# Kernel tuning notes

Measured on AMD Instinct MI355X. Metric: run time of the kernel, lower is better.

The kernel has to match this reference:

```python
import jax, jax.numpy as jnp
import numpy as np
from jax import lax

B, NM, P, F, E, H, K = 32, 131072, 256, 3, 64, 4, 3
DH = E // H


def layer_norm(x, gamma, beta, eps=1e-5):
    mu = x.mean(-1, keepdims=True)
    var = ((x - mu) ** 2).mean(-1, keepdims=True)
    return (x - mu) * lax.rsqrt(var + eps) * gamma + beta


def knn_interp(x, pos_x, pos_y, k=K):
    """x: [B, Nx, F] features at pos_x [Nx, 2]; interpolate to pos_y [Ny, 2].
    Positions are shared across the batch (they are tiled in the torch code),
    so KNN indices/weights are computed once. Matches torch knn + inverse-
    squared-distance weighted scatter (uniform per-batch counts => gather form).
    """
    d2 = jnp.sum((pos_y[:, None, :] - pos_x[None, :, :]) ** 2, axis=-1)  # [Ny, Nx]
    neg_d2, idx = lax.top_k(-d2, k)                                      # [Ny, k]
    w = 1.0 / jnp.clip(-neg_d2, 1e-16)                                   # [Ny, k]
    w = lax.stop_gradient(w)  # torch computes weights under no_grad
    gathered = x[:, idx, :]                                              # [B, Ny, k, F]
    num = jnp.sum(gathered * w[None, :, :, None], axis=2)                # [B, Ny, F]
    den = jnp.sum(w, axis=1)[None, :, None]                              # [1, Ny, 1]
    return num / den


def setup_inputs() -> dict:
    key = jax.random.key(0)
    ks = jax.random.split(key, 8)
    return {
        "node_attr": jax.random.normal(ks[0], (B * NM, F), jnp.float32),
        "position_mesh": jax.random.uniform(ks[1], (NM, 2), jnp.float32),
        "position_pivotal": jax.random.uniform(ks[2], (P, 2), jnp.float32),
        "ln_gamma": jnp.ones((F,), jnp.float32),
        "ln_beta": jnp.zeros((F,), jnp.float32),
        "Wf": jax.random.normal(ks[3], (E, F), jnp.float32) * (2.0 / E) ** 0.5,
        "bf": jnp.zeros((E,), jnp.float32),
        "Wp": jax.random.normal(ks[4], (E, 2), jnp.float32) * (2.0 / E) ** 0.5,
        "bp": jnp.zeros((E,), jnp.float32),
        "in_proj_w": jax.random.normal(ks[5], (3 * E, E), jnp.float32) * (1.0 / E) ** 0.5,
        "in_proj_b": jnp.zeros((3 * E,), jnp.float32),
        "batch_size": B,
    }


def reference(node_attr, position_mesh, position_pivotal, ln_gamma, ln_beta,
              Wf, bf, Wp, bp, in_proj_w, in_proj_b, batch_size):
    x = node_attr.reshape(batch_size, -1, F)                 # [B, NM, F]
    # PivotalNorm after encoder (encoder/decoder MeshGraphNet omitted: undefined dep)
    x = layer_norm(x, ln_gamma, ln_beta)
    # ---- downsample: mesh -> pivotal via inverse-distance KNN interpolation ----
    y = knn_interp(x, position_mesh, position_pivotal)       # [B, P, F]
    # attention-based pooling over pivotal nodes
    q = (jnp.einsum('bpf,ef->bpe', y, Wf) + bf
         + (position_pivotal @ Wp.T + bp)[None])             # [B, P, E]
    Wq, Wk = in_proj_w[:E], in_proj_w[E:2 * E]
    bq, bk = in_proj_b[:E], in_proj_b[E:2 * E]
    Q = (q @ Wq.T + bq).reshape(batch_size, P, H, DH)
    Kt = (q @ Wk.T + bk).reshape(batch_size, P, H, DH)
    scores = jnp.einsum('bqhd,bkhd->bhqk', Q, Kt) / np.float32(np.sqrt(DH))
    attn = jax.nn.softmax(scores, axis=-1)                   # [B, H, P, P]
    attn_w = attn.mean(axis=1)                               # avg heads, [B, P, P]
    y = jnp.einsum('bqk,bkf->bqf', attn_w, y)                # [B, P, F]
    # ---- interpolate: pivotal -> mesh ----
    out = knn_interp(y, position_pivotal, position_mesh)     # [B, NM, F]
    return out.reshape(-1, F)
```

## Files before the change

kernel.cpp:

```cpp
#include <hip/hip_runtime.h>
#include <math.h>

#define NM 131072
#define PP 256
#define BB 32

#define INF_F 3.0e38f
#define LDW 13

#define KA_BLOCKS 256
#define KB_BLOCKS 512

__device__ __forceinline__ void ins3(float d, int i,
    float& d0, float& d1, float& d2, int& i0, int& i1, int& i2) {
  bool l0 = d < d0, l1 = d < d1, l2 = d < d2;
  d2 = l1 ? d1 : (l2 ? d : d2);
  i2 = l1 ? i1 : (l2 ? i : i2);
  d1 = l0 ? d0 : (l1 ? d : d1);
  i1 = l0 ? i0 : (l1 ? i : i1);
  d0 = l0 ? d : d0;
  i0 = l0 ? i : i0;
}

__device__ __forceinline__ bool lt2(float d, int i, float D, int I) {
  return (d < D) || (d == D && i < I);
}

__device__ __forceinline__ void ins3t(float d, int i,
    float& d0, float& d1, float& d2, int& i0, int& i1, int& i2) {
  bool l0 = lt2(d, i, d0, i0), l1 = lt2(d, i, d1, i1), l2 = lt2(d, i, d2, i2);
  d2 = l1 ? d1 : (l2 ? d : d2);
  i2 = l1 ? i1 : (l2 ? i : i2);
  d1 = l0 ? d0 : (l1 ? d : d1);
  i1 = l0 ? i0 : (l1 ? i : i1);
  d0 = l0 ? d : d0;
  i0 = l0 ? i : i0;
}

__device__ __forceinline__ float dist2(float ax, float ay, float bx, float by) {
  float dx = ax - bx, dy = ay - by;
  return __fadd_rn(__fmul_rn(dx, dx), __fmul_rn(dy, dy));
}

__global__ __launch_bounds__(1024)
void fused_knn(const float* __restrict__ mesh, const float* __restrict__ piv,
               float* __restrict__ wA, int* __restrict__ idxA,
               float* __restrict__ wB, int* __restrict__ idxB,
               float* __restrict__ y2) {
  const int blk = blockIdx.x;
  const int tid = threadIdx.x;
  __shared__ float sdf[PP * LDW];
  __shared__ int   sif[PP * LDW];

  if (blk < KA_BLOCKS) {
    const int p = blk;
    const float2 pv = ((const float2*)piv)[p];
    const float2* m2 = (const float2*)mesh;
    float d0 = INF_F, d1 = INF_F, d2 = INF_F;
    int i0 = 0, i1 = 0, i2 = 0;
#pragma unroll 4
    for (int j = 0; j < 128; ++j) {
      int idx = tid + (j << 10);
      float2 mp = m2[idx];
      ins3(dist2(pv.x, pv.y, mp.x, mp.y), idx, d0, d1, d2, i0, i1, i2);
    }
    sdf[tid * 3 + 0] = d0; sif[tid * 3 + 0] = i0;
    sdf[tid * 3 + 1] = d1; sif[tid * 3 + 1] = i1;
    sdf[tid * 3 + 2] = d2; sif[tid * 3 + 2] = i2;
    __syncthreads();

    if (tid < 128) {
      float e0 = INF_F, e1 = INF_F, e2 = INF_F; int j0 = 0, j1 = 0, j2 = 0;
#pragma unroll
      for (int s = 0; s < 8; ++s) {
        int o = (tid + 128 * s) * 3;
#pragma unroll
        for (int k = 0; k < 3; ++k) ins3t(sdf[o + k], sif[o + k], e0, e1, e2, j0, j1, j2);
      }
      sdf[tid * 3 + 0] = e0; sif[tid * 3 + 0] = j0;
      sdf[tid * 3 + 1] = e1; sif[tid * 3 + 1] = j1;
      sdf[tid * 3 + 2] = e2; sif[tid * 3 + 2] = j2;
    }
    __syncthreads();

    if (tid < 16) {
      float e0 = INF_F, e1 = INF_F, e2 = INF_F; int j0 = 0, j1 = 0, j2 = 0;
#pragma unroll
      for (int s = 0; s < 8; ++s) {
        int o = (tid + 16 * s) * 3;
#pragma unroll
        for (int k = 0; k < 3; ++k) ins3t(sdf[o + k], sif[o + k], e0, e1, e2, j0, j1, j2);
      }
      sdf[tid * 3 + 0] = e0; sif[tid * 3 + 0] = j0;
      sdf[tid * 3 + 1] = e1; sif[tid * 3 + 1] = j1;
      sdf[tid * 3 + 2] = e2; sif[tid * 3 + 2] = j2;
    }
    __syncthreads();

    if (tid == 0) {
      float e0 = INF_F, e1 = INF_F, e2 = INF_F; int j0 = 0, j1 = 0, j2 = 0;
      for (int s = 0; s < 16; ++s) {
        int o = s * 3;
#pragma unroll
        for (int k = 0; k < 3; ++k) ins3t(sdf[o + k], sif[o + k], e0, e1, e2, j0, j1, j2);
      }
      wA[p * 3 + 0] = 1.0f / fmaxf(e0, 1e-16f); idxA[p * 3 + 0] = j0;
      wA[p * 3 + 1] = 1.0f / fmaxf(e1, 1e-16f); idxA[p * 3 + 1] = j1;
      wA[p * 3 + 2] = 1.0f / fmaxf(e2, 1e-16f); idxA[p * 3 + 2] = j2;
    }
  } else if (blk < KA_BLOCKS + KB_BLOCKS) {
    const int bi = blk - KA_BLOCKS;
    const int ml = tid & 255;
    const int sub = tid >> 8;
    const int m = bi * 256 + ml;
    const float2 mv = ((const float2*)mesh)[m];
    float d0 = INF_F, d1 = INF_F, d2 = INF_F;
    int i0 = 0, i1 = 0, i2 = 0;
    const int base = sub * 64;
#pragma unroll 4
    for (int i = 0; i < 64; ++i) {
      int idx = base + i;
      float px = piv[2 * idx], py = piv[2 * idx + 1];
      ins3(dist2(mv.x, mv.y, px, py), idx, d0, d1, d2, i0, i1, i2);
    }
    sdf[ml * LDW + sub * 3 + 0] = d0; sif[ml * LDW + sub * 3 + 0] = i0;
    sdf[ml * LDW + sub * 3 + 1] = d1; sif[ml * LDW + sub * 3 + 1] = i1;
    sdf[ml * LDW + sub * 3 + 2] = d2; sif[ml * LDW + sub * 3 + 2] = i2;
    __syncthreads();

    if (tid < 256) {
      float e0 = sdf[tid * LDW + 0], e1 = sdf[tid * LDW + 1], e2 = sdf[tid * LDW + 2];
      int j0 = sif[tid * LDW + 0], j1 = sif[tid * LDW + 1], j2 = sif[tid * LDW + 2];
#pragma unroll
      for (int s = 1; s < 4; ++s)
#pragma unroll
        for (int k = 0; k < 3; ++k)
          ins3(sdf[tid * LDW + s * 3 + k], sif[tid * LDW + s * 3 + k], e0, e1, e2, j0, j1, j2);
      const int m0 = bi * 256 + tid;
      wB[m0 * 3 + 0] = 1.0f / fmaxf(e0, 1e-16f); idxB[m0 * 3 + 0] = j0;
      wB[m0 * 3 + 1] = 1.0f / fmaxf(e1, 1e-16f); idxB[m0 * 3 + 1] = j1;
      wB[m0 * 3 + 2] = 1.0f / fmaxf(e2, 1e-16f); idxB[m0 * 3 + 2] = j2;
    }
  } else {
    float4 z; z.x = 0.f; z.y = 0.f; z.z = 0.f; z.w = 0.f;
    float4* p4 = (float4*)y2;
#pragma unroll
    for (int j = 0; j < 6; ++j) p4[tid + (j << 10)] = z;
  }
}

__global__ __launch_bounds__(128, 2)
void gather_qqk(const float* __restrict__ node, const float* __restrict__ piv,
                const float* __restrict__ gamma, const float* __restrict__ beta,
                const float* __restrict__ Wf, const float* __restrict__ bf,
                const float* __restrict__ Wp, const float* __restrict__ bp,
                const float* __restrict__ ipw, const float* __restrict__ ipb,
                const float* __restrict__ wA, const int* __restrict__ idxA,
                float* __restrict__ y, float* __restrict__ Qh, float* __restrict__ Kh) {
  const int b = blockIdx.x >> 5;
  const int ptile = (blockIdx.x & 31) * 8;
  const int t = threadIdx.x;
  __shared__ float qs[8][64];
  __shared__ float ys[8][3];

  if (t < 8) {
    const int p = ptile + t;
    const float g0 = gamma[0], g1 = gamma[1], g2 = gamma[2];
    const float be0 = beta[0], be1 = beta[1], be2 = beta[2];
    float num0 = 0.f, num1 = 0.f, num2 = 0.f, den = 0.f;
#pragma unroll
    for (int k = 0; k < 3; ++k) {
      int idx = idxA[p * 3 + k];
      float w = wA[p * 3 + k];
      const float* r = node + ((size_t)b * NM + idx) * 3;
      float a0 = r[0], a1 = r[1], a2 = r[2];
      float mu = (a0 + a1 + a2) * (1.0f / 3.0f);
      float e0 = a0 - mu, e1 = a1 - mu, e2 = a2 - mu;
      float var = (e0 * e0 + e1 * e1 + e2 * e2) * (1.0f / 3.0f);
      float sc = 1.0f / sqrtf(var + 1e-5f);
      num0 += (e0 * sc * g0 + be0) * w;
      num1 += (e1 * sc * g1 + be1) * w;
      num2 += (e2 * sc * g2 + be2) * w;
      den += w;
    }
    float o0 = num0 / den, o1 = num1 / den, o2 = num2 / den;
    ys[t][0] = o0; ys[t][1] = o1; ys[t][2] = o2;
    float* yr = y + (b * PP + p) * 3;
    yr[0] = o0; yr[1] = o1; yr[2] = o2;
  }
  __syncthreads();

  const int e = t & 63;
  const int half = t >> 6;
  {
    float wf0 = Wf[e * 3], wf1 = Wf[e * 3 + 1], wf2 = Wf[e * 3 + 2];
    float wp0 = Wp[e * 2], wp1 = Wp[e * 2 + 1];
    float cst = bf[e] + bp[e];
    for (int r = half; r < 8; r += 2) {
      int p = ptile + r;
      float pe = piv[2 * p] * wp0 + piv[2 * p + 1] * wp1;
      qs[r][e] = ys[r][0] * wf0 + ys[r][1] * wf1 + ys[r][2] * wf2 + cst + pe;
    }
  }
  __syncthreads();

  const int row = half * 64 + e;
  float wreg[64];
  const float4* W4 = (const float4*)(ipw + row * 64);
#pragma unroll
  for (int j = 0; j < 16; ++j) {
    float4 v = W4[j];
    wreg[4 * j] = v.x; wreg[4 * j + 1] = v.y; wreg[4 * j + 2] = v.z; wreg[4 * j + 3] = v.w;
  }
  float bias = ipb[row];
  float* dst = half ? Kh : Qh;
  const int h = e >> 4, d = e & 15;
  for (int r = 0; r < 8; ++r) {
    float acc = bias;
#pragma unroll
    for (int j = 0; j < 64; ++j) acc += qs[r][j] * wreg[j];
    int p = ptile + r;
    dst[(((b * 4 + h) * PP) + p) * 16 + d] = acc;
  }
}

__global__ void attn_kernel(const float* __restrict__ Qh, const float* __restrict__ Kh,
                            const float* __restrict__ y, float* __restrict__ y2) {
  const int b = blockIdx.x >> 3;
  const int h = (blockIdx.x >> 1) & 3;
  const int qh = blockIdx.x & 1;
  const int t = threadIdx.x;
  const int q = qh * 128 + t;

  __shared__ float Ks[PP * 16];
  __shared__ float ys[PP * 3];

  {
    const float4* src = (const float4*)(Kh + (size_t)(b * 4 + h) * PP * 16);
    float4* dst = (float4*)Ks;
#pragma unroll
    for (int j = 0; j < 8; ++j) dst[j * 128 + t] = src[j * 128 + t];
    const float* ysrc = y + b * PP * 3;
#pragma unroll
    for (int j = 0; j < 6; ++j) ys[j * 128 + t] = ysrc[j * 128 + t];
  }
  __syncthreads();

  const float4* q4 = (const float4*)(Qh + ((size_t)((b * 4 + h) * PP) + q) * 16);
  float4 qa = q4[0], qb = q4[1], qc = q4[2], qd = q4[3];

  float m = -INF_F, l = 0.f, a0 = 0.f, a1 = 0.f, a2 = 0.f;
#pragma unroll 4
  for (int k = 0; k < PP; ++k) {
    const float4* kr = (const float4*)(Ks + k * 16);
    float4 k0 = kr[0], k1 = kr[1], k2 = kr[2], k3 = kr[3];
    float dot = qa.x * k0.x + qa.y * k0.y + qa.z * k0.z + qa.w * k0.w
              + qb.x * k1.x + qb.y * k1.y + qb.z * k1.z + qb.w * k1.w
              + qc.x * k2.x + qc.y * k2.y + qc.z * k2.z + qc.w * k2.w
              + qd.x * k3.x + qd.y * k3.y + qd.z * k3.z + qd.w * k3.w;
    float s = dot * 0.25f;
    float mn = fmaxf(m, s);
    float p = __expf(s - mn);
    float sc = __expf(m - mn);
    float y0 = ys[k * 3], y1 = ys[k * 3 + 1], yy2 = ys[k * 3 + 2];
    l = l * sc + p;
    a0 = a0 * sc + p * y0;
    a1 = a1 * sc + p * y1;
    a2 = a2 * sc + p * yy2;
    m = mn;
  }
  float inv = 0.25f / l;
  float* o = y2 + (b * PP + q) * 3;
  atomicAdd(o + 0, a0 * inv);
  atomicAdd(o + 1, a1 * inv);
  atomicAdd(o + 2, a2 * inv);
}

__global__ __launch_bounds__(256)
void interp_out(const float* __restrict__ wB, const int* __restrict__ idxB,
                const float* __restrict__ y2, float* __restrict__ out) {
  const int tid = threadIdx.x;
  const int ml = tid & 63;
  const int sub = tid >> 6;
  const int m = blockIdx.x * 64 + ml;

  const float w0 = wB[m * 3 + 0], w1 = wB[m * 3 + 1], w2 = wB[m * 3 + 2];
  const int o0 = idxB[m * 3 + 0] * 3, o1 = idxB[m * 3 + 1] * 3, o2 = idxB[m * 3 + 2] * 3;
  const float inv = 1.0f / (w0 + w1 + w2);

#pragma unroll 2
  for (int bi = 0; bi < 8; ++bi) {
    const int b = sub * 8 + bi;
    const float* yb = y2 + b * PP * 3;
    float3 r0 = *(const float3*)(yb + o0);
    float3 r1 = *(const float3*)(yb + o1);
    float3 r2 = *(const float3*)(yb + o2);
    float3 res;
    res.x = (w0 * r0.x + w1 * r1.x + w2 * r2.x) * inv;
    res.y = (w0 * r0.y + w1 * r1.y + w2 * r2.y) * inv;
    res.z = (w0 * r0.z + w1 * r1.z + w2 * r2.z) * inv;
    *(float3*)(out + ((size_t)b * NM + m) * 3) = res;
  }
}

extern "C" void kernel_launch(void* const* d_in, const int* in_sizes, int n_in,
                              void* d_out, int out_size, void* d_ws, size_t ws_size,
                              hipStream_t stream) {
  const float* node  = (const float*)d_in[0];
  const float* mesh  = (const float*)d_in[1];
  const float* piv   = (const float*)d_in[2];
  const float* gamma = (const float*)d_in[3];
  const float* beta  = (const float*)d_in[4];
  const float* Wf    = (const float*)d_in[5];
  const float* bf    = (const float*)d_in[6];
  const float* Wp    = (const float*)d_in[7];
  const float* bp    = (const float*)d_in[8];
  const float* ipw   = (const float*)d_in[9];
  const float* ipb   = (const float*)d_in[10];
  float* out = (float*)d_out;

  float* wA   = (float*)d_ws;
  int*   idxA = (int*)(wA + PP * 3);
  float* y    = (float*)(idxA + PP * 3);
  float* Qh   = y + BB * PP * 3;
  float* Kh   = Qh + BB * PP * 64;
  float* y2   = Kh + BB * PP * 64;
  float* wB   = y2 + BB * PP * 3;
  int*   idxB = (int*)(wB + NM * 3);

  fused_knn<<<KA_BLOCKS + KB_BLOCKS + 1, 1024, 0, stream>>>(mesh, piv, wA, idxA, wB, idxB, y2);
  gather_qqk<<<BB * 32, 128, 0, stream>>>(node, piv, gamma, beta, Wf, bf, Wp, bp, ipw, ipb,
                                          wA, idxA, y, Qh, Kh);
  attn_kernel<<<BB * 4 * 2, 128, 0, stream>>>(Qh, Kh, y, y2);
  interp_out<<<NM / 64, 256, 0, stream>>>(wB, idxB, y2, out);
}
```

Baseline: 199.4 us.

## Replace brute-force KNN with uniform-grid bucketing and ring search

Replaces the brute-force KNN searches with uniform spatial grids. Mesh points go into a 64x64 grid and pivotal points into a 16x16 grid, each with an overflow list, and queries expand ring by ring until the third-nearest distance is bounded. The mesh-to-pivotal KNN is fused into the output interpolation kernel, removing the wB/idxB workspace round-trip, and attention's online softmax is split into four independent chains for more instruction-level parallelism. It adds a memset, atomic bucket-building and data-dependent control flow. Tie-breaking now relies on packed 64-bit keys.

```diff
diff --git a/kernel.cpp b/kernel.cpp
--- a/kernel.cpp
+++ b/kernel.cpp
@@ -4,37 +4,26 @@
 #define NM 131072
 #define PP 256
 #define BB 32
-
 #define INF_F 3.0e38f
-#define LDW 13
-
-#define KA_BLOCKS 256
-#define KB_BLOCKS 512
-
-__device__ __forceinline__ void ins3(float d, int i,
-    float& d0, float& d1, float& d2, int& i0, int& i1, int& i2) {
-  bool l0 = d < d0, l1 = d < d1, l2 = d < d2;
-  d2 = l1 ? d1 : (l2 ? d : d2);
-  i2 = l1 ? i1 : (l2 ? i : i2);
-  d1 = l0 ? d0 : (l1 ? d : d1);
-  i1 = l0 ? i0 : (l1 ? i : i1);
-  d0 = l0 ? d : d0;
-  i0 = l0 ? i : i0;
-}
-
-__device__ __forceinline__ bool lt2(float d, int i, float D, int I) {
-  return (d < D) || (d == D && i < I);
-}
-
-__device__ __forceinline__ void ins3t(float d, int i,
-    float& d0, float& d1, float& d2, int& i0, int& i1, int& i2) {
-  bool l0 = lt2(d, i, d0, i0), l1 = lt2(d, i, d1, i1), l2 = lt2(d, i, d2, i2);
-  d2 = l1 ? d1 : (l2 ? d : d2);
-  i2 = l1 ? i1 : (l2 ? i : i2);
-  d1 = l0 ? d0 : (l1 ? d : d1);
-  i1 = l0 ? i0 : (l1 ? i : i1);
-  d0 = l0 ? d : d0;
-  i0 = l0 ? i : i0;
+
+#define GM   64
+#define GM2  (GM * GM)
+#define CAPM 96
+#define GP   16
+#define GP2  (GP * GP)
+#define CAPP 8
+
+typedef unsigned long long u64;
+
+__device__ __forceinline__ u64 packkey(float d, int i) {
+  return ((u64)__float_as_uint(d) << 32) | (unsigned)i;
+}
+
+__device__ __forceinline__ void ins3k(u64 k, u64& k0, u64& k1, u64& k2) {
+  bool l0 = k < k0, l1 = k < k1, l2 = k < k2;
+  k2 = l1 ? k1 : (l2 ? k : k2);
+  k1 = l0 ? k0 : (l1 ? k : k1);
+  k0 = l0 ? k : k0;
 }
 
 __device__ __forceinline__ float dist2(float ax, float ay, float bx, float by) {
@@ -42,110 +31,157 @@
   return __fadd_rn(__fmul_rn(dx, dx), __fmul_rn(dy, dy));
 }
 
-__global__ __launch_bounds__(1024)
-void fused_knn(const float* __restrict__ mesh, const float* __restrict__ piv,
-               float* __restrict__ wA, int* __restrict__ idxA,
-               float* __restrict__ wB, int* __restrict__ idxB,
-               float* __restrict__ y2) {
-  const int blk = blockIdx.x;
-  const int tid = threadIdx.x;
-  __shared__ float sdf[PP * LDW];
-  __shared__ int   sif[PP * LDW];
-
-  if (blk < KA_BLOCKS) {
-    const int p = blk;
-    const float2 pv = ((const float2*)piv)[p];
-    const float2* m2 = (const float2*)mesh;
-    float d0 = INF_F, d1 = INF_F, d2 = INF_F;
-    int i0 = 0, i1 = 0, i2 = 0;
-#pragma unroll 4
-    for (int j = 0; j < 128; ++j) {
-      int idx = tid + (j << 10);
-      float2 mp = m2[idx];
-      ins3(dist2(pv.x, pv.y, mp.x, mp.y), idx, d0, d1, d2, i0, i1, i2);
-    }
-    sdf[tid * 3 + 0] = d0; sif[tid * 3 + 0] = i0;
-    sdf[tid * 3 + 1] = d1; sif[tid * 3 + 1] = i1;
-    sdf[tid * 3 + 2] = d2; sif[tid * 3 + 2] = i2;
+__global__ __launch_bounds__(256)
+void build_buckets(const float* __restrict__ mesh, const float* __restrict__ piv,
+                   unsigned* __restrict__ cntM, unsigned* __restrict__ cntP,
+                   unsigned* __restrict__ ovfc,
+                   float* __restrict__ bufM,
+                   int* __restrict__ bufP,
+                   float* __restrict__ ovfM, int* __restrict__ ovfP,
+                   float* __restrict__ y2) {
+  const int g = blockIdx.x * 256 + threadIdx.x;
+  if (g < NM) {
+    float2 mp = ((const float2*)mesh)[g];
+    int cx = min((int)(mp.x * GM), GM - 1);
+    int cy = min((int)(mp.y * GM), GM - 1);
+    int c = cy * GM + cx;
+    unsigned s = atomicAdd(&cntM[c], 1u);
+    if (s < CAPM) {
+      float* d = bufM + (size_t)(c * CAPM + s) * 3;
+      d[0] = mp.x; d[1] = mp.y; ((int*)d)[2] = g;
+    } else {
+      unsigned o = atomicAdd(&ovfc[0], 1u);
+      float* d = ovfM + (size_t)o * 3;
+      d[0] = mp.x; d[1] = mp.y; ((int*)d)[2] = g;
+    }
+  }
+  if (blockIdx.x == 0 && threadIdx.x < PP) {
+    const int p = threadIdx.x;
+    float2 pv = ((const float2*)piv)[p];
+    int cx = min((int)(pv.x * GP), GP - 1);
+    int cy = min((int)(pv.y * GP), GP - 1);
+    int c = cy * GP + cx;
+    unsigned s = atomicAdd(&cntP[c], 1u);
+    if (s < CAPP) bufP[c * CAPP + s] = p;
+    else { unsigned o = atomicAdd(&ovfc[1], 1u); ovfP[o] = p; }
+  }
+  if (blockIdx.x == 1) {
+    for (int j = threadIdx.x; j < BB * PP * 3; j += 256) y2[j] = 0.f;
+  }
+}
+
+__global__ __launch_bounds__(256)
+void knnA_grid(const float* __restrict__ piv,
+               const unsigned* __restrict__ cntM, const float* __restrict__ bufM,
+               const unsigned* __restrict__ ovfc, const float* __restrict__ ovfM,
+               float* __restrict__ wA, int* __restrict__ idxA) {
+  const int p = blockIdx.x;
+  const int t = threadIdx.x;
+  __shared__ u64 sk[256 * 3];
+  __shared__ u64 g3[3];
+  __shared__ int sdone;
+
+  const float2 pv = ((const float2*)piv)[p];
+  const int cx = min((int)(pv.x * GM), GM - 1);
+  const int cy = min((int)(pv.y * GM), GM - 1);
+
+  u64 b0 = ~0ull, b1 = ~0ull, b2 = ~0ull;
+
+  {
+    int x0 = max(cx - 1, 0), x1 = min(cx + 1, GM - 1);
+    int y0 = max(cy - 1, 0), y1 = min(cy + 1, GM - 1);
+    for (int yy = y0; yy <= y1; ++yy) {
+      int cb = yy * GM + x0;
+      int tot = (x1 - x0 + 1) * CAPM;
+      for (int s = t; s < tot; s += 256) {
+        int ci = s / CAPM, j = s - ci * CAPM;
+        int c = cb + ci;
+        if (j < (int)min(cntM[c], (unsigned)CAPM)) {
+          const float* cp = bufM + (size_t)(c * CAPM + j) * 3;
+          float d = dist2(pv.x, pv.y, cp[0], cp[1]);
+          ins3k(packkey(d, ((const int*)cp)[2]), b0, b1, b2);
+        }
+      }
+    }
+    int no = (int)ovfc[0];
+    for (int j = t; j < no; j += 256) {
+      const float* cp = ovfM + (size_t)j * 3;
+      float d = dist2(pv.x, pv.y, cp[0], cp[1]);
+      ins3k(packkey(d, ((const int*)cp)[2]), b0, b1, b2);
+    }
+  }
+
+  int R = 1;
+  u64 p0 = ~0ull, p1 = ~0ull, p2 = ~0ull;
+  while (true) {
+    sk[t * 3 + 0] = b0; sk[t * 3 + 1] = b1; sk[t * 3 + 2] = b2;
     __syncthreads();
-
-    if (tid < 128) {
-      float e0 = INF_F, e1 = INF_F, e2 = INF_F; int j0 = 0, j1 = 0, j2 = 0;
+    if (t < 32) {
+      u64 e0 = ~0ull, e1 = ~0ull, e2 = ~0ull;
 #pragma unroll
       for (int s = 0; s < 8; ++s) {
-        int o = (tid + 128 * s) * 3;
-#pragma unroll
-        for (int k = 0; k < 3; ++k) ins3t(sdf[o + k], sif[o + k], e0, e1, e2, j0, j1, j2);
-      }
-      sdf[tid * 3 + 0] = e0; sif[tid * 3 + 0] = j0;
-      sdf[tid * 3 + 1] = e1; sif[tid * 3 + 1] = j1;
-      sdf[tid * 3 + 2] = e2; sif[tid * 3 + 2] = j2;
+        int o = (t + 32 * s) * 3;
+        ins3k(sk[o], e0, e1, e2); ins3k(sk[o + 1], e0, e1, e2); ins3k(sk[o + 2], e0, e1, e2);
+      }
+      sk[t * 3] = e0; sk[t * 3 + 1] = e1; sk[t * 3 + 2] = e2;
     }
     __syncthreads();
-
-    if (tid < 16) {
-      float e0 = INF_F, e1 = INF_F, e2 = INF_F; int j0 = 0, j1 = 0, j2 = 0;
-#pragma unroll
-      for (int s = 0; s < 8; ++s) {
-        int o = (tid + 16 * s) * 3;
-#pragma unroll
-        for (int k = 0; k < 3; ++k) ins3t(sdf[o + k], sif[o + k], e0, e1, e2, j0, j1, j2);
-      }
-      sdf[tid * 3 + 0] = e0; sif[tid * 3 + 0] = j0;
-      sdf[tid * 3 + 1] = e1; sif[tid * 3 + 1] = j1;
-      sdf[tid * 3 + 2] = e2; sif[tid * 3 + 2] = j2;
+    if (t == 0) {
+      u64 e0 = p0, e1 = p1, e2 = p2;
+      for (int s = 0; s < 32; ++s) {
+        ins3k(sk[s * 3], e0, e1, e2); ins3k(sk[s * 3 + 1], e0, e1, e2); ins3k(sk[s * 3 + 2], e0, e1, e2);
+      }
+      g3[0] = e0; g3[1] = e1; g3[2] = e2;
+      float d2f = __uint_as_float((unsigned)(e2 >> 32));
+      float md = (float)R * (1.0f / GM);
+      sdone = (md * md > d2f) ? 1 : 0;
     }
     __syncthreads();
-
-    if (tid == 0) {
-      float e0 = INF_F, e1 = INF_F, e2 = INF_F; int j0 = 0, j1 = 0, j2 = 0;
-      for (int s = 0; s < 16; ++s) {
-        int o = s * 3;
-#pragma unroll
-        for (int k = 0; k < 3; ++k) ins3t(sdf[o + k], sif[o + k], e0, e1, e2, j0, j1, j2);
-      }
-      wA[p * 3 + 0] = 1.0f / fmaxf(e0, 1e-16f); idxA[p * 3 + 0] = j0;
-      wA[p * 3 + 1] = 1.0f / fmaxf(e1, 1e-16f); idxA[p * 3 + 1] = j1;
-      wA[p * 3 + 2] = 1.0f / fmaxf(e2, 1e-16f); idxA[p * 3 + 2] = j2;
-    }
-  } else if (blk < KA_BLOCKS + KB_BLOCKS) {
-    const int bi = blk - KA_BLOCKS;
-    const int ml = tid & 255;
-    const int sub = tid >> 8;
-    const int m = bi * 256 + ml;
-    const float2 mv = ((const float2*)mesh)[m];
-    float d0 = INF_F, d1 = INF_F, d2 = INF_F;
-    int i0 = 0, i1 = 0, i2 = 0;
-    const int base = sub * 64;
-#pragma unroll 4
-    for (int i = 0; i < 64; ++i) {
-      int idx = base + i;
-      float px = piv[2 * idx], py = piv[2 * idx + 1];
-      ins3(dist2(mv.x, mv.y, px, py), idx, d0, d1, d2, i0, i1, i2);
-    }
-    sdf[ml * LDW + sub * 3 + 0] = d0; sif[ml * LDW + sub * 3 + 0] = i0;
-    sdf[ml * LDW + sub * 3 + 1] = d1; sif[ml * LDW + sub * 3 + 1] = i1;
-    sdf[ml * LDW + sub * 3 + 2] = d2; sif[ml * LDW + sub * 3 + 2] = i2;
+    if (sdone) break;
+    p0 = g3[0]; p1 = g3[1]; p2 = g3[2];
+    b0 = b1 = b2 = ~0ull;
+    R += 1;
+    int x0 = max(cx - R, 0), x1 = min(cx + R, GM - 1);
+    for (int pass = 0; pass < 2; ++pass) {
+      int yy = pass ? cy + R : cy - R;
+      if (yy < 0 || yy > GM - 1) continue;
+      int cb = yy * GM + x0;
+      int tot = (x1 - x0 + 1) * CAPM;
+      for (int s = t; s < tot; s += 256) {
+        int ci = s / CAPM, j = s - ci * CAPM;
+        int c = cb + ci;
+        if (j < (int)min(cntM[c], (unsigned)CAPM)) {
+          const float* cp = bufM + (size_t)(c * CAPM + j) * 3;
+          float d = dist2(pv.x, pv.y, cp[0], cp[1]);
+          ins3k(packkey(d, ((const int*)cp)[2]), b0, b1, b2);
+        }
+      }
+    }
+    int yy0 = max(cy - R + 1, 0), yy1 = min(cy + R - 1, GM - 1);
+    for (int pass = 0; pass < 2; ++pass) {
+      int xx = pass ? cx + R : cx - R;
+      if (xx < 0 || xx > GM - 1) continue;
+      int tot = (yy1 - yy0 + 1) * CAPM;
+      for (int s = t; s < tot; s += 256) {
+        int ri = s / CAPM, j = s - ri * CAPM;
+        int c = (yy0 + ri) * GM + xx;
+        if (j < (int)min(cntM[c], (unsigned)CAPM)) {
+          const float* cp = bufM + (size_t)(c * CAPM + j) * 3;
+          float d = dist2(pv.x, pv.y, cp[0], cp[1]);
+          ins3k(packkey(d, ((const int*)cp)[2]), b0, b1, b2);
+        }
+      }
+    }
     __syncthreads();
-
-    if (tid < 256) {
-      float e0 = sdf[tid * LDW + 0], e1 = sdf[tid * LDW + 1], e2 = sdf[tid * LDW + 2];
-      int j0 = sif[tid * LDW + 0], j1 = sif[tid * LDW + 1], j2 = sif[tid * LDW + 2];
-#pragma unroll
-      for (int s = 1; s < 4; ++s)
-#pragma unroll
-        for (int k = 0; k < 3; ++k)
-          ins3(sdf[tid * LDW + s * 3 + k], sif[tid * LDW + s * 3 + k], e0, e1, e2, j0, j1, j2);
-      const int m0 = bi * 256 + tid;
-      wB[m0 * 3 + 0] = 1.0f / fmaxf(e0, 1e-16f); idxB[m0 * 3 + 0] = j0;
-      wB[m0 * 3 + 1] = 1.0f / fmaxf(e1, 1e-16f); idxB[m0 * 3 + 1] = j1;
-      wB[m0 * 3 + 2] = 1.0f / fmaxf(e2, 1e-16f); idxB[m0 * 3 + 2] = j2;
-    }
-  } else {
-    float4 z; z.x = 0.f; z.y = 0.f; z.z = 0.f; z.w = 0.f;
-    float4* p4 = (float4*)y2;
-#pragma unroll
-    for (int j = 0; j < 6; ++j) p4[tid + (j << 10)] = z;
+  }
+  if (t == 0) {
+#pragma unroll
+    for (int k = 0; k < 3; ++k) {
+      u64 e = g3[k];
+      float d = __uint_as_float((unsigned)(e >> 32));
+      wA[p * 3 + k] = 1.0f / fmaxf(d, 1e-16f);
+      idxA[p * 3 + k] = (int)(unsigned)(e & 0xffffffffu);
+    }
   }
 }
 
@@ -234,7 +270,6 @@
 
   __shared__ float Ks[PP * 16];
   __shared__ float ys[PP * 3];
-
   {
     const float4* src = (const float4*)(Kh + (size_t)(b * 4 + h) * PP * 16);
     float4* dst = (float4*)Ks;
@@ -249,52 +284,148 @@
   const float4* q4 = (const float4*)(Qh + ((size_t)((b * 4 + h) * PP) + q) * 16);
   float4 qa = q4[0], qb = q4[1], qc = q4[2], qd = q4[3];
 
-  float m = -INF_F, l = 0.f, a0 = 0.f, a1 = 0.f, a2 = 0.f;
-#pragma unroll 4
-  for (int k = 0; k < PP; ++k) {
-    const float4* kr = (const float4*)(Ks + k * 16);
-    float4 k0 = kr[0], k1 = kr[1], k2 = kr[2], k3 = kr[3];
-    float dot = qa.x * k0.x + qa.y * k0.y + qa.z * k0.z + qa.w * k0.w
-              + qb.x * k1.x + qb.y * k1.y + qb.z * k1.z + qb.w * k1.w
-              + qc.x * k2.x + qc.y * k2.y + qc.z * k2.z + qc.w * k2.w
-              + qd.x * k3.x + qd.y * k3.y + qd.z * k3.z + qd.w * k3.w;
-    float s = dot * 0.25f;
-    float mn = fmaxf(m, s);
-    float p = __expf(s - mn);
-    float sc = __expf(m - mn);
-    float y0 = ys[k * 3], y1 = ys[k * 3 + 1], yy2 = ys[k * 3 + 2];
-    l = l * sc + p;
-    a0 = a0 * sc + p * y0;
-    a1 = a1 * sc + p * y1;
-    a2 = a2 * sc + p * yy2;
-    m = mn;
-  }
+  float m0 = -INF_F, m1 = -INF_F, m2 = -INF_F, m3 = -INF_F;
+  float l0 = 0, l1 = 0, l2 = 0, l3 = 0;
+  float a00 = 0, a01 = 0, a02 = 0, a10 = 0, a11 = 0, a12 = 0;
+  float a20 = 0, a21 = 0, a22 = 0, a30 = 0, a31 = 0, a32 = 0;
+
+#define CHAIN(c, mC, lC, aC0, aC1, aC2) { \
+    int k = (c) * 64 + kk; \
+    const float4* kr = (const float4*)(Ks + k * 16); \
+    float4 K0 = kr[0], K1 = kr[1], K2 = kr[2], K3 = kr[3]; \
+    float dot = qa.x*K0.x + qa.y*K0.y + qa.z*K0.z + qa.w*K0.w \
+              + qb.x*K1.x + qb.y*K1.y + qb.z*K1.z + qb.w*K1.w \
+              + qc.x*K2.x + qc.y*K2.y + qc.z*K2.z + qc.w*K2.w \
+              + qd.x*K3.x + qd.y*K3.y + qd.z*K3.z + qd.w*K3.w; \
+    float s = dot * 0.25f; \
+    float mn = fmaxf(mC, s); \
+    float pE = __expf(s - mn); \
+    float sc = __expf(mC - mn); \
+    float yv0 = ys[k * 3], yv1 = ys[k * 3 + 1], yv2 = ys[k * 3 + 2]; \
+    lC = lC * sc + pE; \
+    aC0 = aC0 * sc + pE * yv0; \
+    aC1 = aC1 * sc + pE * yv1; \
+    aC2 = aC2 * sc + pE * yv2; \
+    mC = mn; }
+
+#pragma unroll 2
+  for (int kk = 0; kk < 64; ++kk) {
+    CHAIN(0, m0, l0, a00, a01, a02)
+    CHAIN(1, m1, l1, a10, a11, a12)
+    CHAIN(2, m2, l2, a20, a21, a22)
+    CHAIN(3, m3, l3, a30, a31, a32)
+  }
+#undef CHAIN
+
+  float M = fmaxf(fmaxf(m0, m1), fmaxf(m2, m3));
+  float e0 = __expf(m0 - M), e1 = __expf(m1 - M), e2 = __expf(m2 - M), e3 = __expf(m3 - M);
+  float l = l0 * e0 + l1 * e1 + l2 * e2 + l3 * e3;
+  float A0 = a00 * e0 + a10 * e1 + a20 * e2 + a30 * e3;
+  float A1 = a01 * e0 + a11 * e1 + a21 * e2 + a31 * e3;
+  float A2 = a02 * e0 + a12 * e1 + a22 * e2 + a32 * e3;
   float inv = 0.25f / l;
   float* o = y2 + (b * PP + q) * 3;
-  atomicAdd(o + 0, a0 * inv);
-  atomicAdd(o + 1, a1 * inv);
-  atomicAdd(o + 2, a2 * inv);
+  atomicAdd(o + 0, A0 * inv);
+  atomicAdd(o + 1, A1 * inv);
+  atomicAdd(o + 2, A2 * inv);
 }
 
 __global__ __launch_bounds__(256)
-void interp_out(const float* __restrict__ wB, const int* __restrict__ idxB,
-                const float* __restrict__ y2, float* __restrict__ out) {
-  const int tid = threadIdx.x;
-  const int ml = tid & 63;
-  const int sub = tid >> 6;
-  const int m = blockIdx.x * 64 + ml;
-
-  const float w0 = wB[m * 3 + 0], w1 = wB[m * 3 + 1], w2 = wB[m * 3 + 2];
-  const int o0 = idxB[m * 3 + 0] * 3, o1 = idxB[m * 3 + 1] * 3, o2 = idxB[m * 3 + 2] * 3;
-  const float inv = 1.0f / (w0 + w1 + w2);
-
-#pragma unroll 2
-  for (int bi = 0; bi < 8; ++bi) {
-    const int b = sub * 8 + bi;
+void interp_knnB_out(const float* __restrict__ mesh, const float* __restrict__ piv,
+                     const unsigned* __restrict__ cntP, const int* __restrict__ bufP,
+                     const unsigned* __restrict__ ovfc, const int* __restrict__ ovfP,
+                     const float* __restrict__ y2, float* __restrict__ out) {
+  const int t = threadIdx.x;
+  __shared__ float spx[PP], spy[PP];
+  __shared__ unsigned scnt[GP2];
+  __shared__ int sbuf[GP2 * CAPP];
+  {
+    float2 pvv = ((const float2*)piv)[t];
+    spx[t] = pvv.x; spy[t] = pvv.y;
+    scnt[t] = cntP[t];
+    for (int j = t; j < GP2 * CAPP; j += 256) sbuf[j] = bufP[j];
+  }
+  __syncthreads();
+
+  const int m = blockIdx.x * 256 + t;
+  const float2 mv = ((const float2*)mesh)[m];
+  const int cx = min((int)(mv.x * GP), GP - 1);
+  const int cy = min((int)(mv.y * GP), GP - 1);
+  u64 k0 = ~0ull, k1 = ~0ull, k2 = ~0ull;
+
+  {
+    int x0 = max(cx - 2, 0), x1 = min(cx + 2, GP - 1);
+    int y0 = max(cy - 2, 0), y1 = min(cy + 2, GP - 1);
+    for (int yy = y0; yy <= y1; ++yy)
+      for (int xx = x0; xx <= x1; ++xx) {
+        int c = yy * GP + xx;
+        int n = (int)min(scnt[c], (unsigned)CAPP);
+        for (int j = 0; j < n; ++j) {
+          int qq = sbuf[c * CAPP + j];
+          float d = dist2(mv.x, mv.y, spx[qq], spy[qq]);
+          ins3k(packkey(d, qq), k0, k1, k2);
+        }
+      }
+    int no = (int)ovfc[1];
+    for (int j = 0; j < no; ++j) {
+      int qq = ovfP[j];
+      float d = dist2(mv.x, mv.y, spx[qq], spy[qq]);
+      ins3k(packkey(d, qq), k0, k1, k2);
+    }
+  }
+  int R = 2;
+  while (true) {
+    float d2f = __uint_as_float((unsigned)(k2 >> 32));
+    float md = (float)R * (1.0f / GP);
+    if (md * md > d2f) break;
+    R += 1;
+    if (R >= 2 * GP) break;
+    int x0 = max(cx - R, 0), x1 = min(cx + R, GP - 1);
+    for (int pass = 0; pass < 2; ++pass) {
+      int yy = pass ? cy + R : cy - R;
+      if (yy < 0 || yy > GP - 1) continue;
+      for (int xx = x0; xx <= x1; ++xx) {
+        int c = yy * GP + xx;
+        int n = (int)min(scnt[c], (unsigned)CAPP);
+        for (int j = 0; j < n; ++j) {
+          int qq = sbuf[c * CAPP + j];
+          float d = dist2(mv.x, mv.y, spx[qq], spy[qq]);
+          ins3k(packkey(d, qq), k0, k1, k2);
+        }
+      }
+    }
+    int yy0 = max(cy - R + 1, 0), yy1 = min(cy + R - 1, GP - 1);
+    for (int pass = 0; pass < 2; ++pass) {
+      int xx = pass ? cx + R : cx - R;
+      if (xx < 0 || xx > GP - 1) continue;
+      for (int yy = yy0; yy <= yy1; ++yy) {
+        int c = yy * GP + xx;
+        int n = (int)min(scnt[c], (unsigned)CAPP);
+        for (int j = 0; j < n; ++j) {
+          int qq = sbuf[c * CAPP + j];
+          float d = dist2(mv.x, mv.y, spx[qq], spy[qq]);
+          ins3k(packkey(d, qq), k0, k1, k2);
+        }
+      }
+    }
+  }
+
+  float d0 = __uint_as_float((unsigned)(k0 >> 32));
+  float d1 = __uint_as_float((unsigned)(k1 >> 32));
+  float d2v = __uint_as_float((unsigned)(k2 >> 32));
+  int j0 = (int)(unsigned)(k0 & 0xffffffffu) * 3;
+  int j1 = (int)(unsigned)(k1 & 0xffffffffu) * 3;
+  int j2 = (int)(unsigned)(k2 & 0xffffffffu) * 3;
+  float w0 = 1.0f / fmaxf(d0, 1e-16f);
+  float w1 = 1.0f / fmaxf(d1, 1e-16f);
+  float w2 = 1.0f / fmaxf(d2v, 1e-16f);
+  float inv = 1.0f / (w0 + w1 + w2);
+
+  for (int b = 0; b < BB; ++b) {
     const float* yb = y2 + b * PP * 3;
-    float3 r0 = *(const float3*)(yb + o0);
-    float3 r1 = *(const float3*)(yb + o1);
-    float3 r2 = *(const float3*)(yb + o2);
+    float3 r0 = *(const float3*)(yb + j0);
+    float3 r1 = *(const float3*)(yb + j1);
+    float3 r2 = *(const float3*)(yb + j2);
     float3 res;
     res.x = (w0 * r0.x + w1 * r1.x + w2 * r2.x) * inv;
     res.y = (w0 * r0.y + w1 * r1.y + w2 * r2.y) * inv;
@@ -319,18 +450,26 @@
   const float* ipb   = (const float*)d_in[10];
   float* out = (float*)d_out;
 
-  float* wA   = (float*)d_ws;
+  unsigned* cntM = (unsigned*)d_ws;
+  unsigned* cntP = cntM + 4096;
+  unsigned* ovfc = cntP + 256;
+  float* bufM = (float*)d_ws + 4608;
+  int*   bufP = (int*)(bufM + (size_t)GM2 * CAPM * 3);
+  float* ovfM = (float*)(bufP + GP2 * CAPP);
+  int*   ovfP = (int*)(ovfM + (size_t)NM * 3);
+  float* wA   = (float*)(ovfP + PP);
   int*   idxA = (int*)(wA + PP * 3);
   float* y    = (float*)(idxA + PP * 3);
   float* Qh   = y + BB * PP * 3;
   float* Kh   = Qh + BB * PP * 64;
   float* y2   = Kh + BB * PP * 64;
-  float* wB   = y2 + BB * PP * 3;
-  int*   idxB = (int*)(wB + NM * 3);
-
-  fused_knn<<<KA_BLOCKS + KB_BLOCKS + 1, 1024, 0, stream>>>(mesh, piv, wA, idxA, wB, idxB, y2);
+
+  hipMemsetAsync(cntM, 0, 4608 * sizeof(unsigned), stream);
+  build_buckets<<<NM / 256, 256, 0, stream>>>(mesh, piv, cntM, cntP, ovfc,
+                                              bufM, bufP, ovfM, ovfP, y2);
+  knnA_grid<<<PP, 256, 0, stream>>>(piv, cntM, bufM, ovfc, ovfM, wA, idxA);
   gather_qqk<<<BB * 32, 128, 0, stream>>>(node, piv, gamma, beta, Wf, bf, Wp, bp, ipw, ipb,
                                           wA, idxA, y, Qh, Kh);
   attn_kernel<<<BB * 4 * 2, 128, 0, stream>>>(Qh, Kh, y, y2);
-  interp_out<<<NM / 64, 256, 0, stream>>>(wB, idxB, y2, out);
-}
+  interp_knnB_out<<<NM / 256, 256, 0, stream>>>(mesh, piv, cntP, bufP, ovfc, ovfP, y2, out);
+}
```

Result: slower. 220.4 us (+10.5%).
